# Kernel optimization log

Measured on AMD Instinct MI355X. Metric: run time of the kernel, lower is better.

Reference implementation:

```python
import jax, jax.numpy as jnp
import numpy as np

N, K, C, SP = 65536, 16, 64, 8
C8 = C // SP  # attn_nn output dim == C // share_planes == 8
E = N * K
EPS = 1e-5


def _bn(x, g, b):
    # BatchNorm1d in training mode: batch statistics over the row dim
    mu = x.mean(0)
    var = ((x - mu) ** 2).mean(0)
    return (x - mu) * jax.lax.rsqrt(var + EPS) * g + b


def _segment_softmax(a, seg, n):
    m = jax.ops.segment_max(a, seg, num_segments=n)
    e = jnp.exp(a - m[seg])
    s = jax.ops.segment_sum(e, seg, num_segments=n)
    return e / s[seg]


def setup_inputs() -> dict:
    key = jax.random.key(0)
    ks = jax.random.split(key, 12)

    def w(k, shape, fan_in):
        return jax.random.normal(k, shape, jnp.float32) / np.sqrt(fan_in).astype(np.float32)

    x = jax.random.normal(ks[0], (N, C), jnp.float32)
    pos = jax.random.uniform(ks[1], (N, 3), jnp.float32)
    src = jax.random.randint(ks[2], (E,), 0, N)          # knn neighbor ids
    dst = jnp.repeat(jnp.arange(N), K)                   # k neighbors per target node
    edge_index = jnp.stack([src, dst]).astype(jnp.int32)
    return dict(
        x=x, pos=pos, edge_index=edge_index,
        W_in=w(ks[3], (C, C), C), W_out=w(ks[4], (C, C), C),
        pos_w1=w(ks[5], (3, 3), 3), pos_b1=jnp.zeros(3, jnp.float32),
        pos_bn_g=jnp.ones(3, jnp.float32), pos_bn_b=jnp.zeros(3, jnp.float32),
        pos_w2=w(ks[6], (C, 3), 3), pos_b2=jnp.zeros(C, jnp.float32),
        attn_bn1_g=jnp.ones(C, jnp.float32), attn_bn1_b=jnp.zeros(C, jnp.float32),
        attn_w1=w(ks[7], (C8, C), C), attn_b1=jnp.zeros(C8, jnp.float32),
        attn_bn2_g=jnp.ones(C8, jnp.float32), attn_bn2_b=jnp.zeros(C8, jnp.float32),
        attn_w2=w(ks[8], (C8, C8), C8), attn_b2=jnp.zeros(C8, jnp.float32),
        lin_w=w(ks[9], (C, C), C), lin_b=jnp.zeros(C, jnp.float32),
        src_w=w(ks[10], (C, C), C), src_b=jnp.zeros(C, jnp.float32),
        dst_w=w(ks[11], (C, C), C), dst_b=jnp.zeros(C, jnp.float32),
        bn1_g=jnp.ones(C, jnp.float32), bn1_b=jnp.zeros(C, jnp.float32),
        bn2_g=jnp.ones(C, jnp.float32), bn2_b=jnp.zeros(C, jnp.float32),
        bn3_g=jnp.ones(C, jnp.float32), bn3_b=jnp.zeros(C, jnp.float32),
    )


def reference(x, pos, edge_index, W_in, W_out, pos_w1, pos_b1, pos_bn_g, pos_bn_b,
              pos_w2, pos_b2, attn_bn1_g, attn_bn1_b, attn_w1, attn_b1,
              attn_bn2_g, attn_bn2_b, attn_w2, attn_b2, lin_w, lin_b,
              src_w, src_b, dst_w, dst_b, bn1_g, bn1_b, bn2_g, bn2_b, bn3_g, bn3_b):
    src, dst = edge_index[0], edge_index[1]
    x_skip = x
    # lin_in + bn1 + relu
    h = jax.nn.relu(_bn(x @ W_in.T, bn1_g, bn1_b))

    # --- PointTransformerConv ---
    a_src = h @ src_w.T + src_b
    a_dst = h @ dst_w.T + dst_b
    hW = h @ lin_w.T + lin_b

    rel = pos[src] - pos[dst]              # pos_j - pos_i  [E,3]
    d = jax.nn.relu(_bn(rel @ pos_w1.T + pos_b1, pos_bn_g, pos_bn_b))
    delta = d @ pos_w2.T + pos_b2          # [E,C]

    a = a_src[src] - a_dst[dst] + delta    # alpha_j - alpha_i + delta  [E,C]
    # attn_nn: BN -> ReLU -> (Lin C->C8, BN, ReLU) -> Lin C8->C8
    a = jax.nn.relu(_bn(a, attn_bn1_g, attn_bn1_b))
    a = jax.nn.relu(_bn(a @ attn_w1.T + attn_b1, attn_bn2_g, attn_bn2_b))
    a = a @ attn_w2.T + attn_b2            # [E,C8]
    alpha = _segment_softmax(a, dst, N)    # softmax over each node's neighborhood

    # grouped weighting with share_planes: [E,SP,C8] * [E,1,C8]
    msg = (alpha[:, None, :] * (hW[src] + delta).reshape(E, SP, C8)).reshape(E, C)
    out = jax.ops.segment_sum(msg, dst, num_segments=N)  # aggr='add'

    h2 = jax.nn.relu(_bn(out, bn2_g, bn2_b))
    h3 = _bn(h2 @ W_out.T, bn3_g, bn3_b)
    return jax.nn.relu(h3 + x_skip)
```

## Files before the change

### kernel.cpp

```cpp
#include <hip/hip_runtime.h>
#include <cstddef>

constexpr int N_ = 65536;
constexpr int K_ = 16;
constexpr int E_ = N_ * K_;
constexpr int C_ = 64;
#define EPS_ 1e-5f
#define SW 68
#define INV_N (1.f / 65536.f)
#define INV_E (1.f / 1048576.f)
#define NSLOT 64

typedef unsigned int uint_t;
typedef float f32x4_t __attribute__((ext_vector_type(4)));
typedef short bf16x8_t __attribute__((ext_vector_type(8)));

__device__ __forceinline__ uint_t bf16_rne(float f) {
    uint_t u = __float_as_uint(f);
    return (u + 0x7fffu + ((u >> 16) & 1u)) >> 16;
}
__device__ __forceinline__ float bf16_lo(uint_t p) { return __uint_as_float(p << 16); }
__device__ __forceinline__ float bf16_hi(uint_t p) { return __uint_as_float(p & 0xffff0000u); }
__device__ __forceinline__ uint_t pk2(float a, float b) {
    return bf16_rne(a) | (bf16_rne(b) << 16);
}
__device__ __forceinline__ uint_t cvtpk(float lo, float hi) {
    uint_t r;
    asm("v_cvt_pk_bf16_f32 %0, %1, %2" : "=v"(r) : "v"(lo), "v"(hi));
    return r;
}

__device__ __forceinline__ void split4(float4 v, uint2& h, uint2& l) {
    h.x = cvtpk(v.x, v.y); h.y = cvtpk(v.z, v.w);
    float r0 = v.x - bf16_lo(h.x), r1 = v.y - bf16_hi(h.x);
    float r2 = v.z - bf16_lo(h.y), r3 = v.w - bf16_hi(h.y);
    l.x = cvtpk(r0, r1); l.y = cvtpk(r2, r3);
}

__device__ __forceinline__ void bn_ss(const float* __restrict__ s, int nchp, int c,
                                      float invM, const float* __restrict__ g,
                                      const float* __restrict__ b,
                                      float& sc, float& sh)
{
    float mean = s[c] * invM;
    float var  = fmaxf(s[nchp + c] * invM - mean * mean, 0.f);
    sc = g[c] * rsqrtf(var + EPS_);
    sh = b[c] - mean * sc;
}

__global__ void k_zero(float* __restrict__ p, int n)
{
    int i = blockIdx.x * 1024 + threadIdx.x;
    if (i < n) p[i] = 0.f;
}

#define TS 36

__device__ __forceinline__ void stage_x_split(const float* __restrict__ in,
                                              const float* __restrict__ ss,
                                              uint_t* __restrict__ Xh,
                                              uint_t* __restrict__ Xl,
                                              int row0, int t)
{
#pragma unroll
    for (int it = 0; it < 4; ++it) {
        int m = t + 256 * it;
        int r = m >> 4, j = m & 15;
        float4 v = ((const float4*)in)[(size_t)(row0 + r) * 16 + j];
        if (ss) {
            float4 sc = ((const float4*)ss)[j];
            float4 sh = ((const float4*)(ss + 64))[j];
            v.x = fmaxf(fmaf(v.x, sc.x, sh.x), 0.f);
            v.y = fmaxf(fmaf(v.y, sc.y, sh.y), 0.f);
            v.z = fmaxf(fmaf(v.z, sc.z, sh.z), 0.f);
            v.w = fmaxf(fmaf(v.w, sc.w, sh.w), 0.f);
        }
        uint2 h, l; split4(v, h, l);
        *(uint2*)&Xh[r * TS + 2 * j] = h;
        *(uint2*)&Xl[r * TS + 2 * j] = l;
    }
}

__device__ __forceinline__ void stage_w_split(const float* __restrict__ W,
                                              uint_t* __restrict__ Wh,
                                              uint_t* __restrict__ Wl, int t)
{
#pragma unroll
    for (int it = 0; it < 4; ++it) {
        int m = t + 256 * it;
        int r = m >> 4, j = m & 15;
        float4 v = ((const float4*)W)[m];
        uint2 h, l; split4(v, h, l);
        *(uint2*)&Wh[r * TS + 2 * j] = h;
        *(uint2*)&Wl[r * TS + 2 * j] = l;
    }
}

struct AFrag { uint4 h0, h1, l0, l1; };

__device__ __forceinline__ AFrag load_afrag(const uint_t* __restrict__ Xh,
                                            const uint_t* __restrict__ Xl,
                                            int L, int wv)
{
    int cl = L & 15, kb = L >> 4;
    int o = (16 * wv + cl) * TS + kb * 4;
    AFrag a;
    a.h0 = *(const uint4*)&Xh[o]; a.h1 = *(const uint4*)&Xh[o + 16];
    a.l0 = *(const uint4*)&Xl[o]; a.l1 = *(const uint4*)&Xl[o + 16];
    return a;
}

#define MF(A, B, C) __builtin_amdgcn_mfma_f32_16x16x32_bf16( \
        *(const bf16x8_t*)&(A), *(const bf16x8_t*)&(B), (C), 0, 0, 0)

__device__ __forceinline__ void mfma_tile(const AFrag& af,
                                          const uint_t* __restrict__ Wh,
                                          const uint_t* __restrict__ Wl,
                                          int L, f32x4_t acc[4])
{
    int cl = L & 15, kb = L >> 4;
#pragma unroll
    for (int ct = 0; ct < 4; ++ct) {
        int o = (ct * 16 + cl) * TS + kb * 4;
        uint4 Bh0 = *(const uint4*)&Wh[o], Bh1 = *(const uint4*)&Wh[o + 16];
        uint4 Bl0 = *(const uint4*)&Wl[o], Bl1 = *(const uint4*)&Wl[o + 16];
        f32x4_t a = {0.f, 0.f, 0.f, 0.f};
        a = MF(af.h0, Bh0, a); a = MF(af.l0, Bh0, a); a = MF(af.h0, Bl0, a);
        a = MF(af.h1, Bh1, a); a = MF(af.l1, Bh1, a); a = MF(af.h1, Bl1, a);
        acc[ct] = a;
    }
}

__device__ __forceinline__ void ytile_store(float* __restrict__ ybuf, int L, int wv,
                                            const f32x4_t acc[4])
{
    int cl = L & 15, kb = L >> 4;
#pragma unroll
    for (int ct = 0; ct < 4; ++ct)
#pragma unroll
        for (int j = 0; j < 4; ++j)
            ybuf[(16 * wv + kb * 4 + j) * SW + ct * 16 + cl] = acc[ct][j];
}

__global__ __launch_bounds__(256)
void k_gemm_tile(const float* __restrict__ in, const float* __restrict__ W,
                 const float* __restrict__ acc_in, const float* __restrict__ g_in,
                 const float* __restrict__ b_in, float invM_in,
                 float* __restrict__ out, float* __restrict__ acc_out)
{
    __shared__ __align__(16) uint_t shb[4 * 64 * TS];
    __shared__ float ssm[128];
    __shared__ float raws[128];
    uint_t* Xh = shb;           uint_t* Xl = shb + 64 * TS;
    uint_t* Wh = shb + 2 * 64 * TS; uint_t* Wl = shb + 3 * 64 * TS;
    float* ybuf = (float*)shb;
    float4* scr = (float4*)((float*)shb + 4352);
    int t = threadIdx.x, L = t & 63, wv = t >> 6;
    int row0 = blockIdx.x * 64;
    if (acc_in) {
        if (t < 128) {
            float s = 0.f;
            for (int sl = 0; sl < NSLOT; ++sl) s += acc_in[sl * 128 + t];
            raws[t] = s;
        }
        __syncthreads();
        if (t < 64) {
            float scv, shv;
            bn_ss(raws, 64, t, invM_in, g_in, b_in, scv, shv);
            ssm[t] = scv; ssm[64 + t] = shv;
        }
    }
    __syncthreads();
    stage_x_split(in, acc_in ? ssm : nullptr, Xh, Xl, row0, t);
    stage_w_split(W, Wh, Wl, t);
    __syncthreads();
    AFrag af = load_afrag(Xh, Xl, L, wv);
    f32x4_t acc[4];
    mfma_tile(af, Wh, Wl, L, acc);
    __syncthreads();
    ytile_store(ybuf, L, wv, acc);
    __syncthreads();
    float s0 = 0, s1 = 0, s2 = 0, s3 = 0, q0 = 0, q1 = 0, q2 = 0, q3 = 0;
#pragma unroll
    for (int it = 0; it < 4; ++it) {
        int m = t + 256 * it;
        int r = m >> 4, j = m & 15;
        float4 v = *(const float4*)&ybuf[r * SW + 4 * j];
        ((float4*)out)[(size_t)(row0 + r) * 16 + j] = v;
        s0 += v.x; q0 = fmaf(v.x, v.x, q0);
        s1 += v.y; q1 = fmaf(v.y, v.y, q1);
        s2 += v.z; q2 = fmaf(v.z, v.z, q2);
        s3 += v.w; q3 = fmaf(v.w, v.w, q3);
    }
    scr[t]       = make_float4(s0, s1, s2, s3);
    scr[256 + t] = make_float4(q0, q1, q2, q3);
    __syncthreads();
    if (t < 16) {
        float4 S = make_float4(0, 0, 0, 0), Q = make_float4(0, 0, 0, 0);
#pragma unroll
        for (int k = 0; k < 16; ++k) {
            float4 a = scr[k * 16 + t], b = scr[256 + k * 16 + t];
            S.x += a.x; S.y += a.y; S.z += a.z; S.w += a.w;
            Q.x += b.x; Q.y += b.y; Q.z += b.z; Q.w += b.w;
        }
        float* ao = acc_out + (blockIdx.x & (NSLOT - 1)) * 128;
        atomicAdd(&ao[4 * t + 0], S.x); atomicAdd(&ao[4 * t + 1], S.y);
        atomicAdd(&ao[4 * t + 2], S.z); atomicAdd(&ao[4 * t + 3], S.w);
        atomicAdd(&ao[64 + 4 * t + 0], Q.x); atomicAdd(&ao[64 + 4 * t + 1], Q.y);
        atomicAdd(&ao[64 + 4 * t + 2], Q.z); atomicAdd(&ao[64 + 4 * t + 3], Q.w);
    }
}

__global__ __launch_bounds__(256)
void k_gemm3_tile(const float* __restrict__ y, const float* __restrict__ acc1,
                  const float* __restrict__ g1, const float* __restrict__ b1,
                  const float* __restrict__ Wa, const float* __restrict__ ba,
                  const float* __restrict__ Wb, const float* __restrict__ bb,
                  const float* __restrict__ Wc, const float* __restrict__ bc,
                  unsigned short* __restrict__ oa16, float* __restrict__ ob,
                  unsigned short* __restrict__ oc16)
{
    __shared__ __align__(16) uint_t shb[4 * 64 * TS];
    __shared__ float ssm[128];
    __shared__ float raws[128];
    uint_t* Xh = shb;           uint_t* Xl = shb + 64 * TS;
    uint_t* Wh = shb + 2 * 64 * TS; uint_t* Wl = shb + 3 * 64 * TS;
    float* ybuf = (float*)shb;
    int t = threadIdx.x, L = t & 63, wv = t >> 6;
    int row0 = blockIdx.x * 64;
    if (t < 128) {
        float s = 0.f;
        for (int sl = 0; sl < NSLOT; ++sl) s += acc1[sl * 128 + t];
        raws[t] = s;
    }
    __syncthreads();
    if (t < 64) {
        float scv, shv;
        bn_ss(raws, 64, t, INV_N, g1, b1, scv, shv);
        ssm[t] = scv; ssm[64 + t] = shv;
    }
    __syncthreads();
    stage_x_split(y, ssm, Xh, Xl, row0, t);
    stage_w_split(Wa, Wh, Wl, t);
    __syncthreads();
    AFrag af = load_afrag(Xh, Xl, L, wv);
    f32x4_t acc[4];
    mfma_tile(af, Wh, Wl, L, acc);
    __syncthreads();
    ytile_store(ybuf, L, wv, acc);
    __syncthreads();
#pragma unroll
    for (int it = 0; it < 4; ++it) {
        int m = t + 256 * it;
        int r = m >> 4, j = m & 15;
        float4 v = *(const float4*)&ybuf[r * SW + 4 * j];
        float4 bv = ((const float4*)ba)[j];
        uint2 o;
        o.x = pk2(v.x + bv.x, v.y + bv.y);
        o.y = pk2(v.z + bv.z, v.w + bv.w);
        ((uint2*)oa16)[(size_t)(row0 + r) * 16 + j] = o;
    }
    __syncthreads();
    stage_w_split(Wb, Wh, Wl, t);
    __syncthreads();
    mfma_tile(af, Wh, Wl, L, acc);
    __syncthreads();
    ytile_store(ybuf, L, wv, acc);
    __syncthreads();
#pragma unroll
    for (int it = 0; it < 4; ++it) {
        int m = t + 256 * it;
        int r = m >> 4, j = m & 15;
        float4 v = *(const float4*)&ybuf[r * SW + 4 * j];
        float4 bv = ((const float4*)bb)[j];
        v.x += bv.x; v.y += bv.y; v.z += bv.z; v.w += bv.w;
        ((float4*)ob)[(size_t)(row0 + r) * 16 + j] = v;
    }
    __syncthreads();
    stage_w_split(Wc, Wh, Wl, t);
    __syncthreads();
    mfma_tile(af, Wh, Wl, L, acc);
    __syncthreads();
    ytile_store(ybuf, L, wv, acc);
    __syncthreads();
#pragma unroll
    for (int it = 0; it < 4; ++it) {
        int m = t + 256 * it;
        int r = m >> 4, j = m & 15;
        float4 v = *(const float4*)&ybuf[r * SW + 4 * j];
        float4 bv = ((const float4*)bc)[j];
        uint2 o;
        o.x = pk2(v.x + bv.x, v.y + bv.y);
        o.y = pk2(v.z + bv.z, v.w + bv.w);
        ((uint2*)oc16)[(size_t)(row0 + r) * 16 + j] = o;
    }
}

__global__ __launch_bounds__(256)
void k_pos_stats(const float* __restrict__ pos, const int* __restrict__ src,
                 const float* __restrict__ pw1, const float* __restrict__ pb1,
                 float* __restrict__ acc)
{
    float s0 = 0, s1 = 0, s2 = 0, q0 = 0, q1 = 0, q2 = 0;
    int tid = blockIdx.x * 256 + threadIdx.x;
    for (int e = tid; e < E_; e += 1024 * 256) {
        int si = src[e], di = e >> 4;
        float rx = pos[3 * si + 0] - pos[3 * di + 0];
        float ry = pos[3 * si + 1] - pos[3 * di + 1];
        float rz = pos[3 * si + 2] - pos[3 * di + 2];
        float u0 = fmaf(rx, pw1[0], fmaf(ry, pw1[1], fmaf(rz, pw1[2], pb1[0])));
        float u1 = fmaf(rx, pw1[3], fmaf(ry, pw1[4], fmaf(rz, pw1[5], pb1[1])));
        float u2 = fmaf(rx, pw1[6], fmaf(ry, pw1[7], fmaf(rz, pw1[8], pb1[2])));
        s0 += u0; q0 = fmaf(u0, u0, q0);
        s1 += u1; q1 = fmaf(u1, u1, q1);
        s2 += u2; q2 = fmaf(u2, u2, q2);
    }
#pragma unroll
    for (int m = 1; m < 64; m <<= 1) {
        s0 += __shfl_xor(s0, m, 64); s1 += __shfl_xor(s1, m, 64); s2 += __shfl_xor(s2, m, 64);
        q0 += __shfl_xor(q0, m, 64); q1 += __shfl_xor(q1, m, 64); q2 += __shfl_xor(q2, m, 64);
    }
    __shared__ float red[4][8];
    int wv = threadIdx.x >> 6, ln = threadIdx.x & 63;
    if (ln == 0) {
        red[wv][0] = s0; red[wv][1] = s1; red[wv][2] = s2; red[wv][3] = 0.f;
        red[wv][4] = q0; red[wv][5] = q1; red[wv][6] = q2; red[wv][7] = 0.f;
    }
    __syncthreads();
    if (threadIdx.x < 8)
        atomicAdd(&acc[(blockIdx.x & (NSLOT - 1)) * 32 + threadIdx.x],
                  red[0][threadIdx.x] + red[1][threadIdx.x] + red[2][threadIdx.x] + red[3][threadIdx.x]);
}

__global__ __launch_bounds__(256)
void k_abn1_stats(const float* __restrict__ pos, const int* __restrict__ src,
                  const unsigned short* __restrict__ asrc16,
                  const float* __restrict__ adst,
                  const float* __restrict__ pw1, const float* __restrict__ pb1,
                  const float* __restrict__ accpos, const float* __restrict__ pbg,
                  const float* __restrict__ pbb, const float* __restrict__ pw2,
                  const float* __restrict__ pb2, float* __restrict__ acc_a1)
{
    __shared__ float rawP[8];
    int t = threadIdx.x;
    int l = t & 15, g = t >> 4, wv = t >> 6;
    int c0 = 4 * l;
    if (t < 8) {
        float s = 0.f;
        for (int sl = 0; sl < NSLOT; ++sl) s += accpos[sl * 32 + t];
        rawP[t] = s;
    }
    __syncthreads();
    float ps0, ph0, ps1, ph1, ps2, ph2;
    bn_ss(rawP, 4, 0, INV_E, pbg, pbb, ps0, ph0);
    bn_ss(rawP, 4, 1, INV_E, pbg, pbb, ps1, ph1);
    bn_ss(rawP, 4, 2, INV_E, pbg, pbb, ps2, ph2);
    float4 p0 = *(const float4*)(pw2 + 12 * l);
    float4 p1 = *(const float4*)(pw2 + 12 * l + 4);
    float4 p2 = *(const float4*)(pw2 + 12 * l + 8);
    float4 pb = *(const float4*)(pb2 + c0);
    float sa0 = 0, sa1 = 0, sa2 = 0, sa3 = 0;
    float qa0 = 0, qa1 = 0, qa2 = 0, qa3 = 0;
#pragma unroll
    for (int nn = 0; nn < 2; ++nn) {
        int n = blockIdx.x * 32 + nn * 16 + g;
        float4 dv = *(const float4*)(adst + (size_t)n * 64 + c0);
        float pnx = pos[3 * n + 0], pny = pos[3 * n + 1], pnz = pos[3 * n + 2];
        int si_l = src[n * 16 + l];
        float rx = pos[3 * si_l + 0] - pnx;
        float ry = pos[3 * si_l + 1] - pny;
        float rz = pos[3 * si_l + 2] - pnz;
        float u0 = fmaf(rx, pw1[0], fmaf(ry, pw1[1], fmaf(rz, pw1[2], pb1[0])));
        float u1 = fmaf(rx, pw1[3], fmaf(ry, pw1[4], fmaf(rz, pw1[5], pb1[1])));
        float u2 = fmaf(rx, pw1[6], fmaf(ry, pw1[7], fmaf(rz, pw1[8], pb1[2])));
        float dl0 = fmaxf(fmaf(u0, ps0, ph0), 0.f);
        float dl1 = fmaxf(fmaf(u1, ps1, ph1), 0.f);
        float dl2 = fmaxf(fmaf(u2, ps2, ph2), 0.f);
        for (int k = 0; k < 16; ++k) {
            int si = __shfl(si_l, k, 16);
            float d0 = __shfl(dl0, k, 16);
            float d1 = __shfl(dl1, k, 16);
            float d2 = __shfl(dl2, k, 16);
            uint2 raw = ((const uint2*)asrc16)[(size_t)si * 16 + l];
            float avx = bf16_lo(raw.x), avy = bf16_hi(raw.x);
            float avz = bf16_lo(raw.y), avw = bf16_hi(raw.y);
            float del0 = fmaf(d0, p0.x, fmaf(d1, p0.y, fmaf(d2, p0.z, pb.x)));
            float del1 = fmaf(d0, p0.w, fmaf(d1, p1.x, fmaf(d2, p1.y, pb.y)));
            float del2 = fmaf(d0, p1.z, fmaf(d1, p1.w, fmaf(d2, p2.x, pb.z)));
            float del3 = fmaf(d0, p2.y, fmaf(d1, p2.z, fmaf(d2, p2.w, pb.w)));
            float a0 = avx - dv.x + del0;
            float a1 = avy - dv.y + del1;
            float a2 = avz - dv.z + del2;
            float a3 = avw - dv.w + del3;
            sa0 += a0; qa0 = fmaf(a0, a0, qa0);
            sa1 += a1; qa1 = fmaf(a1, a1, qa1);
            sa2 += a2; qa2 = fmaf(a2, a2, qa2);
            sa3 += a3; qa3 = fmaf(a3, a3, qa3);
        }
    }
#pragma unroll
    for (int m = 16; m <= 32; m <<= 1) {
        sa0 += __shfl_xor(sa0, m, 64); sa1 += __shfl_xor(sa1, m, 64);
        sa2 += __shfl_xor(sa2, m, 64); sa3 += __shfl_xor(sa3, m, 64);
        qa0 += __shfl_xor(qa0, m, 64); qa1 += __shfl_xor(qa1, m, 64);
        qa2 += __shfl_xor(qa2, m, 64); qa3 += __shfl_xor(qa3, m, 64);
    }
    __shared__ float red[4][128];
    if ((t & 63) < 16) {
        red[wv][c0 + 0] = sa0; red[wv][c0 + 1] = sa1;
        red[wv][c0 + 2] = sa2; red[wv][c0 + 3] = sa3;
        red[wv][64 + c0 + 0] = qa0; red[wv][64 + c0 + 1] = qa1;
        red[wv][64 + c0 + 2] = qa2; red[wv][64 + c0 + 3] = qa3;
    }
    __syncthreads();
    if (t < 128)
        atomicAdd(&acc_a1[(blockIdx.x & (NSLOT - 1)) * 128 + t],
                  red[0][t] + red[1][t] + red[2][t] + red[3][t]);
}

__global__ __launch_bounds__(256)
void k_edge_t1(const float* __restrict__ pos, const int* __restrict__ src,
               const unsigned short* __restrict__ asrc16,
               const float* __restrict__ adst,
               const float* __restrict__ pw1, const float* __restrict__ pb1,
               const float* __restrict__ accpos, const float* __restrict__ pbg,
               const float* __restrict__ pbb, const float* __restrict__ pw2,
               const float* __restrict__ pb2, const float* __restrict__ acc_a1,
               const float* __restrict__ a1g, const float* __restrict__ a1b,
               const float* __restrict__ aw1, const float* __restrict__ ab1,
               float* __restrict__ t1, float* __restrict__ acc_a2)
{
    __shared__ uint2 an_lds[4096];
    float* shf = (float*)an_lds;
    char*  anb = (char*)an_lds;
    int t = threadIdx.x;
    int l = t & 15, g = t >> 4, wv = t >> 6;
    int L = t & 63;
    int c0 = 4 * l;
    if (t < 128) {
        float s = 0.f;
        for (int sl = 0; sl < NSLOT; ++sl) s += acc_a1[sl * 128 + t];
        shf[t] = s;
    } else if (t < 136) {
        int i = t - 128;
        float s = 0.f;
        for (int sl = 0; sl < NSLOT; ++sl) s += accpos[sl * 32 + i];
        shf[128 + i] = s;
    }
    __syncthreads();
    float ps0, ph0, ps1, ph1, ps2, ph2;
    bn_ss(shf + 128, 4, 0, INV_E, pbg, pbb, ps0, ph0);
    bn_ss(shf + 128, 4, 1, INV_E, pbg, pbb, ps1, ph1);
    bn_ss(shf + 128, 4, 2, INV_E, pbg, pbb, ps2, ph2);
    float scx, shx, scy, shy, scz, shz, scw, shw;
    bn_ss(shf, 64, c0 + 0, INV_E, a1g, a1b, scx, shx);
    bn_ss(shf, 64, c0 + 1, INV_E, a1g, a1b, scy, shy);
    bn_ss(shf, 64, c0 + 2, INV_E, a1g, a1b, scz, shz);
    bn_ss(shf, 64, c0 + 3, INV_E, a1g, a1b, scw, shw);
    float4 p0 = *(const float4*)(pw2 + 12 * l);
    float4 p1 = *(const float4*)(pw2 + 12 * l + 4);
    float4 p2 = *(const float4*)(pw2 + 12 * l + 8);
    float4 pb = *(const float4*)(pb2 + c0);
    float Pa0 = p0.x * scx, Pa1 = p0.y * scx, Pa2 = p0.z * scx;
    float Pb0 = p0.w * scy, Pb1 = p1.x * scy, Pb2 = p1.y * scy;
    float Pc0 = p1.z * scz, Pc1 = p1.w * scz, Pc2 = p2.x * scz;
    float Pd0 = p2.y * scw, Pd1 = p2.z * scw, Pd2 = p2.w * scw;
    float qb0 = fmaf(pb.x, scx, shx);
    float qb1 = fmaf(pb.y, scy, shy);
    float qb2 = fmaf(pb.z, scz, shz);
    float qb3 = fmaf(pb.w, scw, shw);
    int col = L & 15, kb = L >> 4;
    uint4 bf0 = make_uint4(0u, 0u, 0u, 0u);
    uint4 bf1 = make_uint4(0u, 0u, 0u, 0u);
    float biasc = 0.f;
    if (col < 8) {
        const float* wr = aw1 + col * 64 + kb * 8;
        bf0 = make_uint4(pk2(wr[0], wr[1]), pk2(wr[2], wr[3]),
                         pk2(wr[4], wr[5]), pk2(wr[6], wr[7]));
        const float* wr2 = wr + 32;
        bf1 = make_uint4(pk2(wr2[0], wr2[1]), pk2(wr2[2], wr2[3]),
                         pk2(wr2[4], wr2[5]), pk2(wr2[6], wr2[7]));
        biasc = ab1[col];
    }
    int ar = col;
    int aoff0 = ar * 128 + ((kb * 16) ^ ((ar & 7) << 4));
    int aoff1 = ar * 128 + ((64 + kb * 16) ^ ((ar & 7) << 4));
    __syncthreads();
    float se = 0.f, sq = 0.f;
#pragma unroll
    for (int nn = 0; nn < 2; ++nn) {
        int n = blockIdx.x * 32 + nn * 16 + g;
        float4 dv = *(const float4*)(adst + (size_t)n * 64 + c0);
        float q0n = fmaf(-dv.x, scx, qb0);
        float q1n = fmaf(-dv.y, scy, qb1);
        float q2n = fmaf(-dv.z, scz, qb2);
        float q3n = fmaf(-dv.w, scw, qb3);
        float pnx = pos[3 * n + 0], pny = pos[3 * n + 1], pnz = pos[3 * n + 2];
        int si_l = src[n * 16 + l];
        float rx = pos[3 * si_l + 0] - pnx;
        float ry = pos[3 * si_l + 1] - pny;
        float rz = pos[3 * si_l + 2] - pnz;
        float u0 = fmaf(rx, pw1[0], fmaf(ry, pw1[1], fmaf(rz, pw1[2], pb1[0])));
        float u1 = fmaf(rx, pw1[3], fmaf(ry, pw1[4], fmaf(rz, pw1[5], pb1[1])));
        float u2 = fmaf(rx, pw1[6], fmaf(ry, pw1[7], fmaf(rz, pw1[8], pb1[2])));
        float dl0 = fmaxf(fmaf(u0, ps0, ph0), 0.f);
        float dl1 = fmaxf(fmaf(u1, ps1, ph1), 0.f);
        float dl2 = fmaxf(fmaf(u2, ps2, ph2), 0.f);
#pragma unroll
        for (int k = 0; k < 16; ++k) {
            int si = __shfl(si_l, k, 16);
            float d0 = __shfl(dl0, k, 16);
            float d1 = __shfl(dl1, k, 16);
            float d2 = __shfl(dl2, k, 16);
            uint2 raw = ((const uint2*)asrc16)[(size_t)si * 16 + l];
            float avx = bf16_lo(raw.x), avy = bf16_hi(raw.x);
            float avz = bf16_lo(raw.y), avw = bf16_hi(raw.y);
            float de0 = fmaf(d0, Pa0, fmaf(d1, Pa1, fmaf(d2, Pa2, q0n)));
            float de1 = fmaf(d0, Pb0, fmaf(d1, Pb1, fmaf(d2, Pb2, q1n)));
            float de2 = fmaf(d0, Pc0, fmaf(d1, Pc1, fmaf(d2, Pc2, q2n)));
            float de3 = fmaf(d0, Pd0, fmaf(d1, Pd1, fmaf(d2, Pd2, q3n)));
            float an0 = fmaxf(fmaf(avx, scx, de0), 0.f);
            float an1 = fmaxf(fmaf(avy, scy, de1), 0.f);
            float an2 = fmaxf(fmaf(avz, scz, de2), 0.f);
            float an3 = fmaxf(fmaf(avw, scw, de3), 0.f);
            int woff = g * 2048 + k * 128 + ((8 * l) ^ ((k & 7) << 4));
            *(uint2*)(anb + woff) = make_uint2(cvtpk(an0, an1), cvtpk(an2, an3));
        }
#pragma unroll
        for (int tt = 0; tt < 4; ++tt) {
            int g2 = (wv << 2) + tt;
            int tb = g2 * 2048;
            uint4 a0 = *(const uint4*)(anb + tb + aoff0);
            uint4 a1v = *(const uint4*)(anb + tb + aoff1);
            f32x4_t acc = {0.f, 0.f, 0.f, 0.f};
            acc = __builtin_amdgcn_mfma_f32_16x16x32_bf16(
                      *(const bf16x8_t*)&a0, *(const bf16x8_t*)&bf0, acc, 0, 0, 0);
            acc = __builtin_amdgcn_mfma_f32_16x16x32_bf16(
                      *(const bf16x8_t*)&a1v, *(const bf16x8_t*)&bf1, acc, 0, 0, 0);
            if (col < 8) {
                int n2 = blockIdx.x * 32 + nn * 16 + g2;
                float* op = t1 + (size_t)(n2 * 16 + kb * 4) * 8 + col;
#pragma unroll
                for (int j = 0; j < 4; ++j) {
                    float v = acc[j] + biasc;
                    op[j * 8] = v;
                    se += v; sq = fmaf(v, v, sq);
                }
            }
        }
    }
    se += __shfl_xor(se, 16, 64); sq += __shfl_xor(sq, 16, 64);
    se += __shfl_xor(se, 32, 64); sq += __shfl_xor(sq, 32, 64);
    __syncthreads();
    if (L < 8) { shf[wv * 16 + col] = se; shf[wv * 16 + 8 + col] = sq; }
    __syncthreads();
    if (t < 16)
        atomicAdd(&acc_a2[(blockIdx.x & (NSLOT - 1)) * 32 + t],
                  shf[t] + shf[16 + t] + shf[32 + t] + shf[48 + t]);
}

__global__ __launch_bounds__(256)
void k_node_aggr(const float* __restrict__ pos, const int* __restrict__ src,
                 const float* __restrict__ t1, const float* __restrict__ acc_a2,
                 const float* __restrict__ a2g, const float* __restrict__ a2b,
                 const float* __restrict__ aw2, const float* __restrict__ ab2,
                 const unsigned short* __restrict__ hw16,
                 const float* __restrict__ accpos, const float* __restrict__ pbg,
                 const float* __restrict__ pbb,
                 const float* __restrict__ pw1, const float* __restrict__ pb1,
                 const float* __restrict__ pw2, const float* __restrict__ pb2,
                 float* __restrict__ out, float* __restrict__ acc_bn2)
{
    __shared__ float alds[16][196];
    __shared__ float ssm2[16];
    __shared__ float rawA2[16];
    __shared__ float rawP[8];
    int t = threadIdx.x, l = t & 15, g = t >> 4;
    int c0 = 4 * l;
    if (t < 16) {
        float s = 0.f;
        for (int sl = 0; sl < NSLOT; ++sl) s += acc_a2[sl * 32 + t];
        rawA2[t] = s;
    } else if (t < 24) {
        int i = t - 16;
        float s = 0.f;
        for (int sl = 0; sl < NSLOT; ++sl) s += accpos[sl * 32 + i];
        rawP[i] = s;
    }
    __syncthreads();
    if (t < 8) {
        float scv, shv;
        bn_ss(rawA2, 8, t, INV_E, a2g, a2b, scv, shv);
        ssm2[t] = scv; ssm2[8 + t] = shv;
    }
    __syncthreads();
    float ps0, ph0, ps1, ph1, ps2, ph2;
    bn_ss(rawP, 4, 0, INV_E, pbg, pbb, ps0, ph0);
    bn_ss(rawP, 4, 1, INV_E, pbg, pbb, ps1, ph1);
    bn_ss(rawP, 4, 2, INV_E, pbg, pbb, ps2, ph2);
    float4 p0 = *(const float4*)(pw2 + 12 * l);
    float4 p1 = *(const float4*)(pw2 + 12 * l + 4);
    float4 p2 = *(const float4*)(pw2 + 12 * l + 8);
    float4 pb = *(const float4*)(pb2 + c0);
    int alof = (l & 1) * 4;
    int n = blockIdx.x * 16 + g;
    int e = n * 16 + l;
    const float4* t4 = (const float4*)(t1 + (size_t)e * 8);
    float4 ta = t4[0], tb = t4[1];
    float tv[8] = {ta.x, ta.y, ta.z, ta.w, tb.x, tb.y, tb.z, tb.w};
    float tn[8];
#pragma unroll
    for (int j = 0; j < 8; ++j)
        tn[j] = fmaxf(fmaf(tv[j], ssm2[j], ssm2[8 + j]), 0.f);
    float al[8];
#pragma unroll
    for (int j = 0; j < 8; ++j) {
        float acc = ab2[j];
#pragma unroll
        for (int i = 0; i < 8; ++i) acc = fmaf(tn[i], aw2[j * 8 + i], acc);
        float m = acc;
#pragma unroll
        for (int msk = 1; msk < 16; msk <<= 1) m = fmaxf(m, __shfl_xor(m, msk, 64));
        float ex = __expf(acc - m);
        float sm = ex;
#pragma unroll
        for (int msk = 1; msk < 16; msk <<= 1) sm += __shfl_xor(sm, msk, 64);
        al[j] = ex / sm;
    }
    *(float4*)&alds[g][l * 12]     = make_float4(al[0], al[1], al[2], al[3]);
    *(float4*)&alds[g][l * 12 + 4] = make_float4(al[4], al[5], al[6], al[7]);
    int silane = src[e];
    float pnx = pos[3 * n + 0], pny = pos[3 * n + 1], pnz = pos[3 * n + 2];
    float rx = pos[3 * silane + 0] - pnx;
    float ry = pos[3 * silane + 1] - pny;
    float rz = pos[3 * silane + 2] - pnz;
    float u0 = fmaf(rx, pw1[0], fmaf(ry, pw1[1], fmaf(rz, pw1[2], pb1[0])));
    float u1 = fmaf(rx, pw1[3], fmaf(ry, pw1[4], fmaf(rz, pw1[5], pb1[1])));
    float u2 = fmaf(rx, pw1[6], fmaf(ry, pw1[7], fmaf(rz, pw1[8], pb1[2])));
    float dl0 = fmaxf(fmaf(u0, ps0, ph0), 0.f);
    float dl1 = fmaxf(fmaf(u1, ps1, ph1), 0.f);
    float dl2 = fmaxf(fmaf(u2, ps2, ph2), 0.f);
    float a0 = 0.f, a1 = 0.f, a2 = 0.f, a3 = 0.f;
#pragma unroll 4
    for (int k = 0; k < 16; ++k) {
        int sk = __shfl(silane, k, 16);
        float d0 = __shfl(dl0, k, 16);
        float d1 = __shfl(dl1, k, 16);
        float d2 = __shfl(dl2, k, 16);
        uint2 raw = ((const uint2*)hw16)[(size_t)sk * 16 + l];
        float hvx = bf16_lo(raw.x), hvy = bf16_hi(raw.x);
        float hvz = bf16_lo(raw.y), hvw = bf16_hi(raw.y);
        float4 alv = *(const float4*)&alds[g][k * 12 + alof];
        float del0 = fmaf(d0, p0.x, fmaf(d1, p0.y, fmaf(d2, p0.z, pb.x)));
        float del1 = fmaf(d0, p0.w, fmaf(d1, p1.x, fmaf(d2, p1.y, pb.y)));
        float del2 = fmaf(d0, p1.z, fmaf(d1, p1.w, fmaf(d2, p2.x, pb.z)));
        float del3 = fmaf(d0, p2.y, fmaf(d1, p2.z, fmaf(d2, p2.w, pb.w)));
        a0 = fmaf(alv.x, hvx + del0, a0);
        a1 = fmaf(alv.y, hvy + del1, a1);
        a2 = fmaf(alv.z, hvz + del2, a2);
        a3 = fmaf(alv.w, hvw + del3, a3);
    }
    *(float4*)(out + (size_t)n * 64 + c0) = make_float4(a0, a1, a2, a3);
    __syncthreads();
    float4* scr = (float4*)&alds[0][0];
    scr[g * 16 + l]       = make_float4(a0, a1, a2, a3);
    scr[256 + g * 16 + l] = make_float4(a0 * a0, a1 * a1, a2 * a2, a3 * a3);
    __syncthreads();
    if (t < 16) {
        float4 S = make_float4(0, 0, 0, 0), Q = make_float4(0, 0, 0, 0);
#pragma unroll
        for (int k = 0; k < 16; ++k) {
            float4 a = scr[k * 16 + t], b = scr[256 + k * 16 + t];
            S.x += a.x; S.y += a.y; S.z += a.z; S.w += a.w;
            Q.x += b.x; Q.y += b.y; Q.z += b.z; Q.w += b.w;
        }
        float* ao = acc_bn2 + (blockIdx.x & (NSLOT - 1)) * 128;
        atomicAdd(&ao[4 * t + 0], S.x); atomicAdd(&ao[4 * t + 1], S.y);
        atomicAdd(&ao[4 * t + 2], S.z); atomicAdd(&ao[4 * t + 3], S.w);
        atomicAdd(&ao[64 + 4 * t + 0], Q.x); atomicAdd(&ao[64 + 4 * t + 1], Q.y);
        atomicAdd(&ao[64 + 4 * t + 2], Q.z); atomicAdd(&ao[64 + 4 * t + 3], Q.w);
    }
}

__global__ __launch_bounds__(256)
void k_final(const float* __restrict__ y3, const float* __restrict__ acc3,
             const float* __restrict__ g3, const float* __restrict__ b3,
             const float* __restrict__ x, float* __restrict__ out)
{
    __shared__ float raws[128];
    __shared__ float ssl[128];
    int t = threadIdx.x;
    if (t < 128) {
        float s = 0.f;
        for (int sl = 0; sl < NSLOT; ++sl) s += acc3[sl * 128 + t];
        raws[t] = s;
    }
    __syncthreads();
    if (t < 64) {
        float scv, shv;
        bn_ss(raws, 64, t, INV_N, g3, b3, scv, shv);
        ssl[t] = scv; ssl[64 + t] = shv;
    }
    __syncthreads();
    int i = blockIdx.x * 256 + t;
    int c4 = i & 15;
    float4 sc = *(const float4*)&ssl[4 * c4];
    float4 sh = *(const float4*)&ssl[64 + 4 * c4];
    float4 v  = ((const float4*)y3)[i];
    float4 xs = ((const float4*)x)[i];
    float4 o;
    o.x = fmaxf(fmaf(v.x, sc.x, sh.x) + xs.x, 0.f);
    o.y = fmaxf(fmaf(v.y, sc.y, sh.y) + xs.y, 0.f);
    o.z = fmaxf(fmaf(v.z, sc.z, sh.z) + xs.z, 0.f);
    o.w = fmaxf(fmaf(v.w, sc.w, sh.w) + xs.w, 0.f);
    ((float4*)out)[i] = o;
}

extern "C" void kernel_launch(void* const* d_in, const int* in_sizes, int n_in,
                              void* d_out, int out_size, void* d_ws, size_t ws_size,
                              hipStream_t stream)
{
    const float* x    = (const float*)d_in[0];
    const float* pos  = (const float*)d_in[1];
    const int*   src  = (const int*)d_in[2];
    const float* W_in = (const float*)d_in[3];
    const float* W_out= (const float*)d_in[4];
    const float* pw1  = (const float*)d_in[5];
    const float* pb1  = (const float*)d_in[6];
    const float* pbg  = (const float*)d_in[7];
    const float* pbb  = (const float*)d_in[8];
    const float* pw2  = (const float*)d_in[9];
    const float* pb2  = (const float*)d_in[10];
    const float* a1g  = (const float*)d_in[11];
    const float* a1b  = (const float*)d_in[12];
    const float* aw1  = (const float*)d_in[13];
    const float* ab1  = (const float*)d_in[14];
    const float* a2g  = (const float*)d_in[15];
    const float* a2b  = (const float*)d_in[16];
    const float* aw2  = (const float*)d_in[17];
    const float* ab2  = (const float*)d_in[18];
    const float* linw = (const float*)d_in[19];
    const float* linb = (const float*)d_in[20];
    const float* srcw = (const float*)d_in[21];
    const float* srcb = (const float*)d_in[22];
    const float* dstw = (const float*)d_in[23];
    const float* dstb = (const float*)d_in[24];
    const float* bn1g = (const float*)d_in[25];
    const float* bn1b = (const float*)d_in[26];
    const float* bn2g = (const float*)d_in[27];
    const float* bn2b = (const float*)d_in[28];
    const float* bn3g = (const float*)d_in[29];
    const float* bn3b = (const float*)d_in[30];
    float* outp = (float*)d_out;

    float* ws = (float*)d_ws;
    const size_t NC = (size_t)N_ * C_;
    float* buf_y     = ws;
    float* buf_adst  = ws + NC;
    unsigned short* asrc16 = (unsigned short*)(ws + 2 * NC);
    unsigned short* hw16   = (unsigned short*)(ws + 2 * NC + NC / 2);
    float* buf_t1    = ws + 3 * NC;
    float* accb      = ws + 3 * NC + (size_t)E_ * 8;
    float* acc_bn1 = accb;
    float* acc_pos = accb + 64 * 128;
    float* acc_a1  = acc_pos + 64 * 32;
    float* acc_a2  = acc_a1 + 64 * 128;
    float* acc_bn2 = acc_a2 + 64 * 32;
    float* acc_bn3 = acc_bn2 + 64 * 128;
    const int ACC_TOTAL = 64 * (128 + 32 + 128 + 32 + 128 + 128);
    float* buf_out = buf_adst;

    k_zero<<<(ACC_TOTAL + 1023) / 1024, 1024, 0, stream>>>(accb, ACC_TOTAL);
    k_gemm_tile<<<1024, 256, 0, stream>>>(x, W_in, nullptr, nullptr, nullptr, 0.f,
                                          buf_y, acc_bn1);
    k_gemm3_tile<<<1024, 256, 0, stream>>>(buf_y, acc_bn1, bn1g, bn1b,
                                           srcw, srcb, dstw, dstb, linw, linb,
                                           asrc16, buf_adst, hw16);
    k_pos_stats<<<1024, 256, 0, stream>>>(pos, src, pw1, pb1, acc_pos);
    k_abn1_stats<<<2048, 256, 0, stream>>>(pos, src, asrc16, buf_adst,
                                           pw1, pb1, acc_pos, pbg, pbb,
                                           pw2, pb2, acc_a1);
    k_edge_t1<<<2048, 256, 0, stream>>>(pos, src, asrc16, buf_adst,
                                        pw1, pb1, acc_pos, pbg, pbb, pw2, pb2,
                                        acc_a1, a1g, a1b, aw1, ab1,
                                        buf_t1, acc_a2);
    k_node_aggr<<<4096, 256, 0, stream>>>(pos, src, buf_t1, acc_a2, a2g, a2b,
                                          aw2, ab2, hw16, acc_pos, pbg, pbb,
                                          pw1, pb1, pw2, pb2, buf_out, acc_bn2);
    k_gemm_tile<<<1024, 256, 0, stream>>>(buf_out, W_out, acc_bn2, bn2g, bn2b, INV_N,
                                          buf_y, acc_bn3);
    k_final<<<(N_ * C_ / 4) / 256, 256, 0, stream>>>(buf_y, acc_bn3, bn3g, bn3b, x, outp);

    (void)in_sizes; (void)n_in; (void)out_size; (void)ws_size;
}
```

Measured before the change: 287.6 us.

## Store edge t1 intermediate in bf16 and batch neighbor gathers before compute

The per-edge t1 buffer (E x 8) is now written as bf16 instead of fp32, halving its write and read traffic between k_edge_t1 and k_node_aggr. In three edge kernels the 16 neighbor gathers are issued up front into a register array so the loads are in flight together rather than interleaved with math. The bias/dst term is folded into the delta fma chain, and the zeroing kernel is replaced with hipMemsetAsync. Rounding t1 to bf16 adds precision loss before the second batch norm and softmax, and the gather arrays raise register pressure.

```diff
diff --git a/kernel.cpp b/kernel.cpp
--- a/kernel.cpp
+++ b/kernel.cpp
@@ -46,12 +46,6 @@
     float var  = fmaxf(s[nchp + c] * invM - mean * mean, 0.f);
     sc = g[c] * rsqrtf(var + EPS_);
     sh = b[c] - mean * sc;
-}
-
-__global__ void k_zero(float* __restrict__ p, int n)
-{
-    int i = blockIdx.x * 1024 + threadIdx.x;
-    if (i < n) p[i] = 0.f;
 }
 
 #define TS 36
@@ -365,6 +359,8 @@
     for (int nn = 0; nn < 2; ++nn) {
         int n = blockIdx.x * 32 + nn * 16 + g;
         float4 dv = *(const float4*)(adst + (size_t)n * 64 + c0);
+        float q0n = pb.x - dv.x, q1n = pb.y - dv.y;
+        float q2n = pb.z - dv.z, q3n = pb.w - dv.w;
         float pnx = pos[3 * n + 0], pny = pos[3 * n + 1], pnz = pos[3 * n + 2];
         int si_l = src[n * 16 + l];
         float rx = pos[3 * si_l + 0] - pnx;
@@ -376,22 +372,24 @@
         float dl0 = fmaxf(fmaf(u0, ps0, ph0), 0.f);
         float dl1 = fmaxf(fmaf(u1, ps1, ph1), 0.f);
         float dl2 = fmaxf(fmaf(u2, ps2, ph2), 0.f);
+        uint2 raws16[16];
+#pragma unroll
         for (int k = 0; k < 16; ++k) {
             int si = __shfl(si_l, k, 16);
+            raws16[k] = ((const uint2*)asrc16)[(size_t)si * 16 + l];
+        }
+#pragma unroll
+        for (int k = 0; k < 16; ++k) {
             float d0 = __shfl(dl0, k, 16);
             float d1 = __shfl(dl1, k, 16);
             float d2 = __shfl(dl2, k, 16);
-            uint2 raw = ((const uint2*)asrc16)[(size_t)si * 16 + l];
+            uint2 raw = raws16[k];
             float avx = bf16_lo(raw.x), avy = bf16_hi(raw.x);
             float avz = bf16_lo(raw.y), avw = bf16_hi(raw.y);
-            float del0 = fmaf(d0, p0.x, fmaf(d1, p0.y, fmaf(d2, p0.z, pb.x)));
-            float del1 = fmaf(d0, p0.w, fmaf(d1, p1.x, fmaf(d2, p1.y, pb.y)));
-            float del2 = fmaf(d0, p1.z, fmaf(d1, p1.w, fmaf(d2, p2.x, pb.z)));
-            float del3 = fmaf(d0, p2.y, fmaf(d1, p2.z, fmaf(d2, p2.w, pb.w)));
-            float a0 = avx - dv.x + del0;
-            float a1 = avy - dv.y + del1;
-            float a2 = avz - dv.z + del2;
-            float a3 = avw - dv.w + del3;
+            float a0 = avx + fmaf(d0, p0.x, fmaf(d1, p0.y, fmaf(d2, p0.z, q0n)));
+            float a1 = avy + fmaf(d0, p0.w, fmaf(d1, p1.x, fmaf(d2, p1.y, q1n)));
+            float a2 = avz + fmaf(d0, p1.z, fmaf(d1, p1.w, fmaf(d2, p2.x, q2n)));
+            float a3 = avw + fmaf(d0, p2.y, fmaf(d1, p2.z, fmaf(d2, p2.w, q3n)));
             sa0 += a0; qa0 = fmaf(a0, a0, qa0);
             sa1 += a1; qa1 = fmaf(a1, a1, qa1);
             sa2 += a2; qa2 = fmaf(a2, a2, qa2);
@@ -428,7 +426,7 @@
                const float* __restrict__ pb2, const float* __restrict__ acc_a1,
                const float* __restrict__ a1g, const float* __restrict__ a1b,
                const float* __restrict__ aw1, const float* __restrict__ ab1,
-               float* __restrict__ t1, float* __restrict__ acc_a2)
+               unsigned short* __restrict__ t1, float* __restrict__ acc_a2)
 {
     __shared__ uint2 an_lds[4096];
     float* shf = (float*)an_lds;
@@ -506,13 +504,18 @@
         float dl0 = fmaxf(fmaf(u0, ps0, ph0), 0.f);
         float dl1 = fmaxf(fmaf(u1, ps1, ph1), 0.f);
         float dl2 = fmaxf(fmaf(u2, ps2, ph2), 0.f);
+        uint2 raws16[16];
 #pragma unroll
         for (int k = 0; k < 16; ++k) {
             int si = __shfl(si_l, k, 16);
+            raws16[k] = ((const uint2*)asrc16)[(size_t)si * 16 + l];
+        }
+#pragma unroll
+        for (int k = 0; k < 16; ++k) {
             float d0 = __shfl(dl0, k, 16);
             float d1 = __shfl(dl1, k, 16);
             float d2 = __shfl(dl2, k, 16);
-            uint2 raw = ((const uint2*)asrc16)[(size_t)si * 16 + l];
+            uint2 raw = raws16[k];
             float avx = bf16_lo(raw.x), avy = bf16_hi(raw.x);
             float avz = bf16_lo(raw.y), avw = bf16_hi(raw.y);
             float de0 = fmaf(d0, Pa0, fmaf(d1, Pa1, fmaf(d2, Pa2, q0n)));
@@ -539,11 +542,11 @@
                       *(const bf16x8_t*)&a1v, *(const bf16x8_t*)&bf1, acc, 0, 0, 0);
             if (col < 8) {
                 int n2 = blockIdx.x * 32 + nn * 16 + g2;
-                float* op = t1 + (size_t)(n2 * 16 + kb * 4) * 8 + col;
+                unsigned short* op = t1 + (size_t)(n2 * 16 + kb * 4) * 8 + col;
 #pragma unroll
                 for (int j = 0; j < 4; ++j) {
                     float v = acc[j] + biasc;
-                    op[j * 8] = v;
+                    op[j * 8] = (unsigned short)bf16_rne(v);
                     se += v; sq = fmaf(v, v, sq);
                 }
             }
@@ -561,7 +564,7 @@
 
 __global__ __launch_bounds__(256)
 void k_node_aggr(const float* __restrict__ pos, const int* __restrict__ src,
-                 const float* __restrict__ t1, const float* __restrict__ acc_a2,
+                 const unsigned short* __restrict__ t1, const float* __restrict__ acc_a2,
                  const float* __restrict__ a2g, const float* __restrict__ a2b,
                  const float* __restrict__ aw2, const float* __restrict__ ab2,
                  const unsigned short* __restrict__ hw16,
@@ -605,9 +608,9 @@
     int alof = (l & 1) * 4;
     int n = blockIdx.x * 16 + g;
     int e = n * 16 + l;
-    const float4* t4 = (const float4*)(t1 + (size_t)e * 8);
-    float4 ta = t4[0], tb = t4[1];
-    float tv[8] = {ta.x, ta.y, ta.z, ta.w, tb.x, tb.y, tb.z, tb.w};
+    uint4 t4 = ((const uint4*)t1)[e];
+    float tv[8] = {bf16_lo(t4.x), bf16_hi(t4.x), bf16_lo(t4.y), bf16_hi(t4.y),
+                   bf16_lo(t4.z), bf16_hi(t4.z), bf16_lo(t4.w), bf16_hi(t4.w)};
     float tn[8];
 #pragma unroll
     for (int j = 0; j < 8; ++j)
@@ -640,14 +643,19 @@
     float dl0 = fmaxf(fmaf(u0, ps0, ph0), 0.f);
     float dl1 = fmaxf(fmaf(u1, ps1, ph1), 0.f);
     float dl2 = fmaxf(fmaf(u2, ps2, ph2), 0.f);
-    float a0 = 0.f, a1 = 0.f, a2 = 0.f, a3 = 0.f;
-#pragma unroll 4
+    uint2 hraw[16];
+#pragma unroll
     for (int k = 0; k < 16; ++k) {
         int sk = __shfl(silane, k, 16);
+        hraw[k] = ((const uint2*)hw16)[(size_t)sk * 16 + l];
+    }
+    float a0 = 0.f, a1 = 0.f, a2 = 0.f, a3 = 0.f;
+#pragma unroll
+    for (int k = 0; k < 16; ++k) {
         float d0 = __shfl(dl0, k, 16);
         float d1 = __shfl(dl1, k, 16);
         float d2 = __shfl(dl2, k, 16);
-        uint2 raw = ((const uint2*)hw16)[(size_t)sk * 16 + l];
+        uint2 raw = hraw[k];
         float hvx = bf16_lo(raw.x), hvy = bf16_hi(raw.x);
         float hvz = bf16_lo(raw.y), hvw = bf16_hi(raw.y);
         float4 alv = *(const float4*)&alds[g][k * 12 + alof];
@@ -759,7 +767,7 @@
     float* buf_adst  = ws + NC;
     unsigned short* asrc16 = (unsigned short*)(ws + 2 * NC);
     unsigned short* hw16   = (unsigned short*)(ws + 2 * NC + NC / 2);
-    float* buf_t1    = ws + 3 * NC;
+    unsigned short* buf_t1 = (unsigned short*)(ws + 3 * NC);
     float* accb      = ws + 3 * NC + (size_t)E_ * 8;
     float* acc_bn1 = accb;
     float* acc_pos = accb + 64 * 128;
@@ -770,7 +778,7 @@
     const int ACC_TOTAL = 64 * (128 + 32 + 128 + 32 + 128 + 128);
     float* buf_out = buf_adst;
 
-    k_zero<<<(ACC_TOTAL + 1023) / 1024, 1024, 0, stream>>>(accb, ACC_TOTAL);
+    hipMemsetAsync(accb, 0, (size_t)ACC_TOTAL * sizeof(float), stream);
     k_gemm_tile<<<1024, 256, 0, stream>>>(x, W_in, nullptr, nullptr, nullptr, 0.f,
                                           buf_y, acc_bn1);
     k_gemm3_tile<<<1024, 256, 0, stream>>>(buf_y, acc_bn1, bn1g, bn1b,
```

New measurement: 303.8 us. +5.6%, slower.
